# Kernel optimization log

Measured on AMD Instinct MI355X. Metric: run time of the kernel, lower is better.

Reference implementation:

```python
import jax, jax.numpy as jnp
import numpy as np

H, D_MODEL, TOPK = 8, 512, 32
D_K = D_MODEL // H


def setup_inputs() -> dict:
    key = jax.random.key(0)
    ks = jax.random.split(key, 12)
    B, LQ, LM = 8, 1024, 4096
    s = 1.0 / np.sqrt(D_MODEL)
    inp = {
        "query": jax.random.normal(ks[0], (B, LQ, D_MODEL), jnp.float32),
        "key": jax.random.normal(ks[1], (B, LM, D_MODEL), jnp.float32),
        "value": jax.random.normal(ks[2], (B, LM, D_MODEL), jnp.float32),
        "Wq": jax.random.normal(ks[3], (D_MODEL, D_MODEL), jnp.float32) * s,
        "bq": jax.random.normal(ks[4], (D_MODEL,), jnp.float32) * s,
        "Wk": jax.random.normal(ks[5], (D_MODEL, D_MODEL), jnp.float32) * s,
        "bk": jax.random.normal(ks[6], (D_MODEL,), jnp.float32) * s,
        "Wv": jax.random.normal(ks[7], (D_MODEL, D_MODEL), jnp.float32) * s,
        "bv": jax.random.normal(ks[8], (D_MODEL,), jnp.float32) * s,
        "Wo": jax.random.normal(ks[9], (D_MODEL, D_MODEL), jnp.float32) * s,
        "bo": jax.random.normal(ks[10], (D_MODEL,), jnp.float32) * s,
    }
    return inp


def reference(query, key, value, Wq, bq, Wk, bk, Wv, bv, Wo, bo):
    B, LQ, _ = query.shape
    LM = key.shape[1]
    # torch Linear: x @ W.T + b
    q = (query @ Wq.T + bq).reshape(B, LQ, H, D_K).transpose(0, 2, 1, 3)  # [B,H,LQ,Dk]
    k = (key @ Wk.T + bk).reshape(B, LM, H, D_K).transpose(0, 2, 1, 3)    # [B,H,LM,Dk]
    v = (value @ Wv.T + bv).reshape(B, LM, H, D_K).transpose(0, 2, 1, 3)  # [B,H,LM,Dk]

    scores = jnp.einsum("bhqd,bhmd->bhqm", q, k) / np.sqrt(D_K)          # [B,H,LQ,LM]
    sel_scores, idx = jax.lax.top_k(scores, TOPK)                          # [B,H,LQ,TOPK]
    # gather selected values: [B,H,LQ,TOPK,Dk]
    sel_v = jnp.take_along_axis(v[:, :, None, :, :], idx[..., None], axis=3)
    p_attn = jax.nn.softmax(sel_scores, axis=-1)                           # dropout: eval mode
    x = jnp.einsum("bhqt,bhqtd->bhqd", p_attn, sel_v)                      # [B,H,LQ,Dk]
    x = x.transpose(0, 2, 1, 3).reshape(B, LQ, H * D_K)
    return x @ Wo.T + bo
```

## Files before the change

### kernel.cpp

```cpp
#include <hip/hip_runtime.h>
#include <math.h>

#define DEV static __device__ __forceinline__

DEV void load8(const float* p, float* v) {
    float4 a = *(const float4*)p;
    float4 b = *(const float4*)(p + 4);
    v[0] = a.x; v[1] = a.y; v[2] = a.z; v[3] = a.w;
    v[4] = b.x; v[5] = b.y; v[6] = b.z; v[7] = b.w;
}

__global__ __launch_bounds__(256) void gemm_nt512(
    const float* __restrict__ A, const float* __restrict__ W,
    const float* __restrict__ bias, float* __restrict__ C)
{
    constexpr int BK = 32, NK = 512;
    __shared__ float As[BK][64 + 4];
    __shared__ float Bs[BK][64 + 4];
    const int bm = blockIdx.y * 64, bn = blockIdx.x * 64;
    const int tid = threadIdx.x;
    const int tx = tid & 15, ty = tid >> 4;
    const int lr = tid >> 2, lk = (tid & 3) * 8;
    float acc[4][4] = {};

    for (int k0 = 0; k0 < NK; k0 += BK) {
        float va[8], vb[8];
        load8(A + (size_t)(bm + lr) * NK + k0 + lk, va);
        load8(W + (size_t)(bn + lr) * NK + k0 + lk, vb);
#pragma unroll
        for (int i = 0; i < 8; ++i) { As[lk + i][lr] = va[i]; Bs[lk + i][lr] = vb[i]; }
        __syncthreads();
#pragma unroll
        for (int kk = 0; kk < BK; ++kk) {
            float4 a4 = *(const float4*)&As[kk][ty * 4];
            float4 b4 = *(const float4*)&Bs[kk][tx * 4];
            float a[4] = {a4.x, a4.y, a4.z, a4.w};
            float b[4] = {b4.x, b4.y, b4.z, b4.w};
#pragma unroll
            for (int i = 0; i < 4; ++i)
#pragma unroll
                for (int j = 0; j < 4; ++j)
                    acc[i][j] = fmaf(a[i], b[j], acc[i][j]);
        }
        __syncthreads();
    }

    float4 bv = *(const float4*)&bias[bn + tx * 4];
    float bvv[4] = {bv.x, bv.y, bv.z, bv.w};
#pragma unroll
    for (int i = 0; i < 4; ++i) {
        size_t row = (size_t)(bm + ty * 4 + i) * NK + bn + tx * 4;
        float4 o;
        o.x = acc[i][0] + bvv[0];
        o.y = acc[i][1] + bvv[1];
        o.z = acc[i][2] + bvv[2];
        o.w = acc[i][3] + bvv[3];
        *(float4*)&C[row] = o;
    }
}

__global__ __launch_bounds__(256) void topk_attn_fused(
    const float* __restrict__ Qf, const float* __restrict__ Kf,
    const float* __restrict__ Vp, float* __restrict__ Xp)
{
    constexpr int LQ = 1024, LM = 4096, DK = 64, D = 512, QT = 32, MT = 64, TK = 32, T = 24;
    __shared__ __align__(16) char smem[17408 + 8704 + 9216];
    float  (*ks)[68]   = (float  (*)[68])(smem);
    float  (*wsel)[33] = (float  (*)[33])(smem);
    int    (*isel)[33] = (int    (*)[33])(smem + 4224);
    float  (*qs)[68]   = (float  (*)[68])(smem + 17408);
    float  (*sc)[72]   = (float  (*)[72])(smem + 17408 + 8704);

    const int tid  = threadIdx.x;
    const int lane = tid & 63;
    const int w    = tid >> 6;
    const int g    = lane >> 3, j = lane & 7;
    const int r    = 8 * w + g;
    const int qt = blockIdx.x, h = blockIdx.y, b = blockIdx.z;

    {
        int rr = tid >> 3, d0 = (tid & 7) * 8;
        const float* src = Qf + ((size_t)(b * LQ + qt * QT + rr) * D + h * DK + d0);
        float4 a = *(const float4*)src;
        float4 c = *(const float4*)(src + 4);
        *(float4*)&qs[rr][d0]     = a;
        *(float4*)&qs[rr][d0 + 4] = c;
    }

    float bv[T]; int bi[T];
#pragma unroll
    for (int t = 0; t < T; ++t) { bv[t] = -INFINITY; bi[t] = 0; }
    float curmin = -INFINITY; int minpos = 0;

    const int qg = tid >> 5, mg = tid & 31;
    __syncthreads();

#pragma unroll 1
    for (int mc = 0; mc < LM; mc += MT) {
        {
            int rr = tid >> 2, d0 = (tid & 3) * 16;
            const float* src = Kf + ((size_t)(b * LM + mc + rr) * D + h * DK + d0);
#pragma unroll
            for (int i = 0; i < 16; i += 4)
                *(float4*)&ks[rr][d0 + i] = *(const float4*)(src + i);
        }
        __syncthreads();

        float acc[4][2] = {};
#pragma unroll
        for (int d = 0; d < DK; d += 4) {
            float4 qa[4], kb[2];
#pragma unroll
            for (int i = 0; i < 4; ++i) qa[i] = *(const float4*)&qs[qg + 8 * i][d];
#pragma unroll
            for (int jj = 0; jj < 2; ++jj) kb[jj] = *(const float4*)&ks[mg + 32 * jj][d];
#pragma unroll
            for (int i = 0; i < 4; ++i)
#pragma unroll
                for (int jj = 0; jj < 2; ++jj) {
                    acc[i][jj] = fmaf(qa[i].x, kb[jj].x, acc[i][jj]);
                    acc[i][jj] = fmaf(qa[i].y, kb[jj].y, acc[i][jj]);
                    acc[i][jj] = fmaf(qa[i].z, kb[jj].z, acc[i][jj]);
                    acc[i][jj] = fmaf(qa[i].w, kb[jj].w, acc[i][jj]);
                }
        }
#pragma unroll
        for (int i = 0; i < 4; ++i)
#pragma unroll
            for (int jj = 0; jj < 2; ++jj)
                sc[qg + 8 * i][mg + 32 * jj] = acc[i][jj] * 0.125f;
        __syncthreads();

#pragma unroll
        for (int c = 0; c < 8; ++c) {
            float v = sc[r][8 * c + j];
            if (v > curmin) {
                int idx = mc + 8 * c + j;
#pragma unroll
                for (int t = 0; t < T; ++t)
                    if (t == minpos) { bv[t] = v; bi[t] = idx; }
                float mv = bv[0]; int mp = 0;
#pragma unroll
                for (int t = 1; t < T; ++t)
                    if (bv[t] < mv) { mv = bv[t]; mp = t; }
                curmin = mv; minpos = mp;
            }
        }
        __syncthreads();
    }

    unsigned cons = 0;
    float m0 = 0.0f;
    double sum_part = 0.0;
#pragma unroll 1
    for (int t32 = 0; t32 < TK; ++t32) {
        float lm = -INFINITY; int li = 0x7fffffff; int lp = -1;
#pragma unroll
        for (int t = 0; t < T; ++t) {
            bool ok = !(cons & (1u << t));
            if (ok && (bv[t] > lm || (bv[t] == lm && bi[t] < li))) {
                lm = bv[t]; li = bi[t]; lp = t;
            }
        }
        float gv = lm; int gi = li;
#pragma unroll
        for (int k = 1; k < 8; k <<= 1) {
            float ov = __shfl_xor(gv, k);
            int   oi = __shfl_xor(gi, k);
            if (ov > gv || (ov == gv && oi < gi)) { gv = ov; gi = oi; }
        }
        if (lp >= 0 && gv == lm && gi == li) cons |= 1u << lp;
        if (t32 == 0) m0 = gv;
        if ((t32 & 7) == j) {
            double e = exp((double)(gv - m0));
            sum_part += e;
            isel[r][t32] = gi;
            wsel[r][t32] = (float)e;
        }
    }
#pragma unroll
    for (int k = 1; k < 8; k <<= 1) sum_part += __shfl_xor(sum_part, k);
    {
        double inv = 1.0 / sum_part;
#pragma unroll
        for (int tt = 0; tt < 4; ++tt) {
            int t = 8 * tt + j;
            wsel[r][t] = (float)((double)wsel[r][t] * inv);
        }
    }
    __syncthreads();

    {
        int rr = tid >> 3, d0 = (tid & 7) * 8;
        float4 a0 = {0, 0, 0, 0}, a1 = {0, 0, 0, 0};
#pragma unroll 1
        for (int t = 0; t < TK; ++t) {
            float ww = wsel[rr][t];
            int mi   = isel[rr][t];
            const float* vp = Vp + ((size_t)(b * LM + mi) * D + h * DK + d0);
            float4 v0 = *(const float4*)vp;
            float4 v1 = *(const float4*)(vp + 4);
            a0.x = fmaf(ww, v0.x, a0.x); a0.y = fmaf(ww, v0.y, a0.y);
            a0.z = fmaf(ww, v0.z, a0.z); a0.w = fmaf(ww, v0.w, a0.w);
            a1.x = fmaf(ww, v1.x, a1.x); a1.y = fmaf(ww, v1.y, a1.y);
            a1.z = fmaf(ww, v1.z, a1.z); a1.w = fmaf(ww, v1.w, a1.w);
        }
        float* xp = Xp + ((size_t)(b * LQ + qt * QT + rr) * D + h * DK + d0);
        *(float4*)xp       = a0;
        *(float4*)(xp + 4) = a1;
    }
}

extern "C" void kernel_launch(void* const* d_in, const int* in_sizes, int n_in,
                              void* d_out, int out_size, void* d_ws, size_t ws_size,
                              hipStream_t stream) {
    const float* query = (const float*)d_in[0];
    const float* key   = (const float*)d_in[1];
    const float* value = (const float*)d_in[2];
    const float* Wq    = (const float*)d_in[3];
    const float* bq    = (const float*)d_in[4];
    const float* Wk    = (const float*)d_in[5];
    const float* bk    = (const float*)d_in[6];
    const float* Wv    = (const float*)d_in[7];
    const float* bv    = (const float*)d_in[8];
    const float* Wo    = (const float*)d_in[9];
    const float* bo    = (const float*)d_in[10];
    float* out = (float*)d_out;

    float* Vp = (float*)d_ws;
    float* Xp = Vp + (size_t)32768 * 512;
    float* Qf = Xp + (size_t)8192 * 512;
    float* Kf = Qf + (size_t)8192 * 512;

    dim3 blk(256);
    gemm_nt512<<<dim3(8, 128), blk, 0, stream>>>(query, Wq, bq, Qf);
    gemm_nt512<<<dim3(8, 512), blk, 0, stream>>>(key,   Wk, bk, Kf);
    gemm_nt512<<<dim3(8, 512), blk, 0, stream>>>(value, Wv, bv, Vp);
    topk_attn_fused<<<dim3(32, 8, 8), blk, 0, stream>>>(Qf, Kf, Vp, Xp);
    gemm_nt512<<<dim3(8, 128), blk, 0, stream>>>(Xp, Wo, bo, out);
}
```

Before: 2.077 ms.

## Read Q via wave-uniform scalar loads and double key tile per iteration

```diff
diff --git a/kernel.cpp b/kernel.cpp
--- a/kernel.cpp
+++ b/kernel.cpp
@@ -63,13 +63,12 @@
     const float* __restrict__ Qf, const float* __restrict__ Kf,
     const float* __restrict__ Vp, float* __restrict__ Xp)
 {
-    constexpr int LQ = 1024, LM = 4096, DK = 64, D = 512, QT = 32, MT = 64, TK = 32, T = 24;
-    __shared__ __align__(16) char smem[17408 + 8704 + 9216];
-    float  (*ks)[68]   = (float  (*)[68])(smem);
-    float  (*wsel)[33] = (float  (*)[33])(smem);
-    int    (*isel)[33] = (int    (*)[33])(smem + 4224);
-    float  (*qs)[68]   = (float  (*)[68])(smem + 17408);
-    float  (*sc)[72]   = (float  (*)[72])(smem + 17408 + 8704);
+    constexpr int LQ = 1024, LM = 4096, DK = 64, D = 512, QT = 32, MT = 128, TK = 32, T = 24;
+    __shared__ __align__(16) char smem[34816];
+    float (*ks)[68]    = (float (*)[68])(smem);
+    float (*sc)[136]   = (float (*)[136])(smem + 17408);
+    float (*wsel)[33]  = (float (*)[33])(smem);
+    int   (*isel)[33]  = (int   (*)[33])(smem + 4224);
 
     const int tid  = threadIdx.x;
     const int lane = tid & 63;
@@ -78,61 +77,58 @@
     const int r    = 8 * w + g;
     const int qt = blockIdx.x, h = blockIdx.y, b = blockIdx.z;
 
-    {
-        int rr = tid >> 3, d0 = (tid & 7) * 8;
-        const float* src = Qf + ((size_t)(b * LQ + qt * QT + rr) * D + h * DK + d0);
-        float4 a = *(const float4*)src;
-        float4 c = *(const float4*)(src + 4);
-        *(float4*)&qs[rr][d0]     = a;
-        *(float4*)&qs[rr][d0 + 4] = c;
-    }
+    const int wu = __builtin_amdgcn_readfirstlane(w);
+    const float* qb = Qf + ((size_t)(b * LQ + qt * QT + 8 * wu) * D + h * DK);
 
     float bv[T]; int bi[T];
 #pragma unroll
     for (int t = 0; t < T; ++t) { bv[t] = -INFINITY; bi[t] = 0; }
     float curmin = -INFINITY; int minpos = 0;
 
-    const int qg = tid >> 5, mg = tid & 31;
-    __syncthreads();
+    const int srr = tid >> 2, sd0 = (tid & 3) * 16;
 
 #pragma unroll 1
     for (int mc = 0; mc < LM; mc += MT) {
-        {
-            int rr = tid >> 2, d0 = (tid & 3) * 16;
-            const float* src = Kf + ((size_t)(b * LM + mc + rr) * D + h * DK + d0);
-#pragma unroll
-            for (int i = 0; i < 16; i += 4)
-                *(float4*)&ks[rr][d0 + i] = *(const float4*)(src + i);
-        }
-        __syncthreads();
-
-        float acc[4][2] = {};
-#pragma unroll
-        for (int d = 0; d < DK; d += 4) {
-            float4 qa[4], kb[2];
-#pragma unroll
-            for (int i = 0; i < 4; ++i) qa[i] = *(const float4*)&qs[qg + 8 * i][d];
-#pragma unroll
-            for (int jj = 0; jj < 2; ++jj) kb[jj] = *(const float4*)&ks[mg + 32 * jj][d];
-#pragma unroll
-            for (int i = 0; i < 4; ++i)
-#pragma unroll
-                for (int jj = 0; jj < 2; ++jj) {
-                    acc[i][jj] = fmaf(qa[i].x, kb[jj].x, acc[i][jj]);
-                    acc[i][jj] = fmaf(qa[i].y, kb[jj].y, acc[i][jj]);
-                    acc[i][jj] = fmaf(qa[i].z, kb[jj].z, acc[i][jj]);
-                    acc[i][jj] = fmaf(qa[i].w, kb[jj].w, acc[i][jj]);
+#pragma unroll
+        for (int p = 0; p < 2; ++p) {
+            const float* src = Kf + ((size_t)(b * LM + mc + 64 * p + srr) * D + h * DK + sd0);
+#pragma unroll
+            for (int i2 = 0; i2 < 16; i2 += 4)
+                *(float4*)&ks[64 * p + srr][sd0 + i2] = *(const float4*)(src + i2);
+        }
+        __syncthreads();
+
+        float acc[8][2] = {};
+#pragma unroll 1
+        for (int dc = 0; dc < DK; dc += 4) {
+            float qv[8][4];
+#pragma unroll
+            for (int i = 0; i < 8; ++i)
+#pragma unroll
+                for (int dd = 0; dd < 4; ++dd)
+                    qv[i][dd] = qb[(size_t)i * D + dc + dd];
+            float k0[4], k1[4];
+            *(float4*)&k0[0] = *(const float4*)&ks[lane][dc];
+            *(float4*)&k1[0] = *(const float4*)&ks[64 + lane][dc];
+#pragma unroll
+            for (int dd = 0; dd < 4; ++dd)
+#pragma unroll
+                for (int i = 0; i < 8; ++i) {
+                    acc[i][0] = fmaf(qv[i][dd], k0[dd], acc[i][0]);
+                    acc[i][1] = fmaf(qv[i][dd], k1[dd], acc[i][1]);
                 }
         }
-#pragma unroll
-        for (int i = 0; i < 4; ++i)
-#pragma unroll
-            for (int jj = 0; jj < 2; ++jj)
-                sc[qg + 8 * i][mg + 32 * jj] = acc[i][jj] * 0.125f;
-        __syncthreads();
-
-#pragma unroll
-        for (int c = 0; c < 8; ++c) {
+        __syncthreads();
+
+#pragma unroll
+        for (int i = 0; i < 8; ++i) {
+            sc[8 * wu + i][lane]      = acc[i][0] * 0.125f;
+            sc[8 * wu + i][64 + lane] = acc[i][1] * 0.125f;
+        }
+        __syncthreads();
+
+#pragma unroll
+        for (int c = 0; c < 16; ++c) {
             float v = sc[r][8 * c + j];
             if (v > curmin) {
                 int idx = mc + 8 * c + j;
```

After: 2.307 ms. +11.0%, slower.

## Replace per-element top-k insertion with threshold filtering and candidate rescoring

Applied to the files above, without the earlier changes.

```diff
diff --git a/kernel.cpp b/kernel.cpp
--- a/kernel.cpp
+++ b/kernel.cpp
@@ -10,15 +10,12 @@
     v[4] = b.x; v[5] = b.y; v[6] = b.z; v[7] = b.w;
 }
 
-__global__ __launch_bounds__(256) void gemm_nt512(
-    const float* __restrict__ A, const float* __restrict__ W,
-    const float* __restrict__ bias, float* __restrict__ C)
+DEV void gemm_body(const float* __restrict__ A, const float* __restrict__ W,
+                   const float* __restrict__ bias, float* __restrict__ C,
+                   int bm, int bn, int tid,
+                   float (*As)[68], float (*Bs)[68])
 {
     constexpr int BK = 32, NK = 512;
-    __shared__ float As[BK][64 + 4];
-    __shared__ float Bs[BK][64 + 4];
-    const int bm = blockIdx.y * 64, bn = blockIdx.x * 64;
-    const int tid = threadIdx.x;
     const int tx = tid & 15, ty = tid >> 4;
     const int lr = tid >> 2, lk = (tid & 3) * 8;
     float acc[4][4] = {};
@@ -45,8 +42,8 @@
         __syncthreads();
     }
 
-    float4 bv = *(const float4*)&bias[bn + tx * 4];
-    float bvv[4] = {bv.x, bv.y, bv.z, bv.w};
+    float4 bvv4 = *(const float4*)&bias[bn + tx * 4];
+    float bvv[4] = {bvv4.x, bvv4.y, bvv4.z, bvv4.w};
 #pragma unroll
     for (int i = 0; i < 4; ++i) {
         size_t row = (size_t)(bm + ty * 4 + i) * NK + bn + tx * 4;
@@ -59,17 +56,45 @@
     }
 }
 
+__global__ __launch_bounds__(256) void gemm_nt512(
+    const float* __restrict__ A, const float* __restrict__ W,
+    const float* __restrict__ bias, float* __restrict__ C)
+{
+    __shared__ float As[32][68];
+    __shared__ float Bs[32][68];
+    gemm_body(A, W, bias, C, blockIdx.y * 64, blockIdx.x * 64, threadIdx.x, As, Bs);
+}
+
+__global__ __launch_bounds__(256) void gemm_qkv(
+    const float* __restrict__ Aq, const float* __restrict__ Ak, const float* __restrict__ Av,
+    const float* __restrict__ Wq, const float* __restrict__ Wk, const float* __restrict__ Wv,
+    const float* __restrict__ bq, const float* __restrict__ bk, const float* __restrict__ bv,
+    float* __restrict__ Cq, float* __restrict__ Ck, float* __restrict__ Cv)
+{
+    __shared__ float As[32][68];
+    __shared__ float Bs[32][68];
+    int yb = blockIdx.y;
+    const float *A, *W, *bias; float* C; int bm;
+    if (yb < 128)      { A = Aq; W = Wq; bias = bq; C = Cq; bm = yb * 64; }
+    else if (yb < 640) { A = Ak; W = Wk; bias = bk; C = Ck; bm = (yb - 128) * 64; }
+    else               { A = Av; W = Wv; bias = bv; C = Cv; bm = (yb - 640) * 64; }
+    gemm_body(A, W, bias, C, bm, blockIdx.x * 64, threadIdx.x, As, Bs);
+}
+
 __global__ __launch_bounds__(256) void topk_attn_fused(
     const float* __restrict__ Qf, const float* __restrict__ Kf,
-    const float* __restrict__ Vp, float* __restrict__ Xp)
+    const float* __restrict__ Vp, float* __restrict__ Xp,
+    unsigned short* __restrict__ gbuf)
 {
-    constexpr int LQ = 1024, LM = 4096, DK = 64, D = 512, QT = 32, MT = 64, TK = 32, T = 24;
-    __shared__ __align__(16) char smem[17408 + 8704 + 9216];
-    float  (*ks)[68]   = (float  (*)[68])(smem);
-    float  (*wsel)[33] = (float  (*)[33])(smem);
-    int    (*isel)[33] = (int    (*)[33])(smem + 4224);
-    float  (*qs)[68]   = (float  (*)[68])(smem + 17408);
-    float  (*sc)[72]   = (float  (*)[72])(smem + 17408 + 8704);
+    constexpr int LQ = 1024, LM = 4096, DK = 64, D = 512, QT = 32, MT = 256, TK = 32, T = 24;
+    constexpr int CAP = 624;
+    __shared__ __align__(16) char smem[69632 + 8704 + 128];
+    float (*ks)[68]   = (float (*)[68])(smem);
+    float (*sc)[264]  = (float (*)[264])(smem + 34816);
+    float (*wsel)[33] = (float (*)[33])(smem);
+    int   (*isel)[33] = (int   (*)[33])(smem + 4224);
+    float (*qs)[68]   = (float (*)[68])(smem + 69632);
+    int*  cnt         = (int*)(smem + 69632 + 8704);
 
     const int tid  = threadIdx.x;
     const int lane = tid & 63;
@@ -77,6 +102,8 @@
     const int g    = lane >> 3, j = lane & 7;
     const int r    = 8 * w + g;
     const int qt = blockIdx.x, h = blockIdx.y, b = blockIdx.z;
+
+    const size_t bb = ((size_t)(((b * 8) + h) * 32 + qt) * 32 + r) * CAP;
 
     {
         int rr = tid >> 3, d0 = (tid & 7) * 8;
@@ -86,67 +113,110 @@
         *(float4*)&qs[rr][d0]     = a;
         *(float4*)&qs[rr][d0 + 4] = c;
     }
-
-    float bv[T]; int bi[T];
-#pragma unroll
-    for (int t = 0; t < T; ++t) { bv[t] = -INFINITY; bi[t] = 0; }
-    float curmin = -INFINITY; int minpos = 0;
-
-    const int qg = tid >> 5, mg = tid & 31;
+    if (tid < 32) cnt[tid] = 0;
+
+    float s0 = -INFINITY, s1 = -INFINITY, s2 = -INFINITY, s3 = -INFINITY;
+    float tau = -INFINITY;
+
+    const int qy = tid >> 5, tx = tid & 31;
+    const int srr = tid >> 2, sd0 = (tid & 3) * 16;
     __syncthreads();
 
 #pragma unroll 1
     for (int mc = 0; mc < LM; mc += MT) {
-        {
-            int rr = tid >> 2, d0 = (tid & 3) * 16;
-            const float* src = Kf + ((size_t)(b * LM + mc + rr) * D + h * DK + d0);
-#pragma unroll
-            for (int i = 0; i < 16; i += 4)
-                *(float4*)&ks[rr][d0 + i] = *(const float4*)(src + i);
-        }
-        __syncthreads();
-
-        float acc[4][2] = {};
-#pragma unroll
-        for (int d = 0; d < DK; d += 4) {
-            float4 qa[4], kb[2];
-#pragma unroll
-            for (int i = 0; i < 4; ++i) qa[i] = *(const float4*)&qs[qg + 8 * i][d];
-#pragma unroll
-            for (int jj = 0; jj < 2; ++jj) kb[jj] = *(const float4*)&ks[mg + 32 * jj][d];
+#pragma unroll
+        for (int p = 0; p < 4; ++p) {
+            const float* src = Kf + ((size_t)(b * LM + mc + 64 * p + srr) * D + h * DK + sd0);
+#pragma unroll
+            for (int i2 = 0; i2 < 16; i2 += 4)
+                *(float4*)&ks[64 * p + srr][sd0 + i2] = *(const float4*)(src + i2);
+        }
+        __syncthreads();
+
+        float acc[4][8] = {};
+#pragma unroll 2
+        for (int dc = 0; dc < DK; dc += 4) {
+            float4 qa[4], kb[8];
+#pragma unroll
+            for (int i = 0; i < 4; ++i) qa[i] = *(const float4*)&qs[qy + 8 * i][dc];
+#pragma unroll
+            for (int jj = 0; jj < 8; ++jj) kb[jj] = *(const float4*)&ks[tx + 32 * jj][dc];
 #pragma unroll
             for (int i = 0; i < 4; ++i)
 #pragma unroll
-                for (int jj = 0; jj < 2; ++jj) {
+                for (int jj = 0; jj < 8; ++jj) {
                     acc[i][jj] = fmaf(qa[i].x, kb[jj].x, acc[i][jj]);
                     acc[i][jj] = fmaf(qa[i].y, kb[jj].y, acc[i][jj]);
                     acc[i][jj] = fmaf(qa[i].z, kb[jj].z, acc[i][jj]);
                     acc[i][jj] = fmaf(qa[i].w, kb[jj].w, acc[i][jj]);
                 }
         }
+        __syncthreads();
+
 #pragma unroll
         for (int i = 0; i < 4; ++i)
 #pragma unroll
-            for (int jj = 0; jj < 2; ++jj)
-                sc[qg + 8 * i][mg + 32 * jj] = acc[i][jj] * 0.125f;
-        __syncthreads();
-
-#pragma unroll
-        for (int c = 0; c < 8; ++c) {
+            for (int jj = 0; jj < 8; ++jj)
+                sc[qy + 8 * i][tx + 32 * jj] = acc[i][jj] * 0.125f;
+        __syncthreads();
+
+#pragma unroll 8
+        for (int c = 0; c < 32; ++c) {
             float v = sc[r][8 * c + j];
-            if (v > curmin) {
-                int idx = mc + 8 * c + j;
-#pragma unroll
-                for (int t = 0; t < T; ++t)
-                    if (t == minpos) { bv[t] = v; bi[t] = idx; }
-                float mv = bv[0]; int mp = 0;
-#pragma unroll
-                for (int t = 1; t < T; ++t)
-                    if (bv[t] < mv) { mv = bv[t]; mp = t; }
-                curmin = mv; minpos = mp;
+            if (v > s3) {
+                if (v > s0)      { s3 = s2; s2 = s1; s1 = s0; s0 = v; }
+                else if (v > s1) { s3 = s2; s2 = s1; s1 = v; }
+                else if (v > s2) { s3 = s2; s2 = v; }
+                else             { s3 = v; }
             }
-        }
-        __syncthreads();
+            if (v > tau) {
+                int pos = atomicAdd(&cnt[r], 1);
+                if (pos < CAP) gbuf[bb + pos] = (unsigned short)(mc + 8 * c + j);
+            }
+            if ((c & 7) == 7) {
+                float t4 = s3;
+                t4 = fminf(t4, __shfl_xor(t4, 1));
+                t4 = fminf(t4, __shfl_xor(t4, 2));
+                t4 = fminf(t4, __shfl_xor(t4, 4));
+                tau = t4;
+            }
+        }
+        __syncthreads();
+    }
+
+    const int nc = min(cnt[r], CAP);
+    float bv[T]; int bi[T];
+#pragma unroll
+    for (int t = 0; t < T; ++t) { bv[t] = -INFINITY; bi[t] = 0; }
+    float curmin = -INFINITY; int minpos = 0, minidx = 0;
+
+#pragma unroll 1
+    for (int p = j; p < nc; p += 8) {
+        int idx = gbuf[bb + p];
+        const float* krow = Kf + ((size_t)(b * LM + idx) * D + h * DK);
+        float a = 0.0f;
+#pragma unroll
+        for (int d = 0; d < DK; d += 4) {
+            float4 k4 = *(const float4*)(krow + d);
+            float4 q4 = *(const float4*)&qs[r][d];
+            a = fmaf(q4.x, k4.x, a);
+            a = fmaf(q4.y, k4.y, a);
+            a = fmaf(q4.z, k4.z, a);
+            a = fmaf(q4.w, k4.w, a);
+        }
+        float v = a * 0.125f;
+
+        bool take = (v > curmin) || (v == curmin && idx < minidx);
+        if (take) {
+#pragma unroll
+            for (int t = 0; t < T; ++t)
+                if (t == minpos) { bv[t] = v; bi[t] = idx; }
+            float mv = bv[0]; int mp = 0, mi = bi[0];
+#pragma unroll
+            for (int t = 1; t < T; ++t)
+                if (bv[t] < mv || (bv[t] == mv && bi[t] > mi)) { mv = bv[t]; mp = t; mi = bi[t]; }
+            curmin = mv; minpos = mp; minidx = mi;
+        }
     }
 
     unsigned cons = 0;
@@ -231,11 +301,12 @@
     float* Xp = Vp + (size_t)32768 * 512;
     float* Qf = Xp + (size_t)8192 * 512;
     float* Kf = Qf + (size_t)8192 * 512;
+    unsigned short* gbuf = (unsigned short*)((char*)d_ws + (size_t)167772160);
 
     dim3 blk(256);
-    gemm_nt512<<<dim3(8, 128), blk, 0, stream>>>(query, Wq, bq, Qf);
-    gemm_nt512<<<dim3(8, 512), blk, 0, stream>>>(key,   Wk, bk, Kf);
-    gemm_nt512<<<dim3(8, 512), blk, 0, stream>>>(value, Wv, bv, Vp);
-    topk_attn_fused<<<dim3(32, 8, 8), blk, 0, stream>>>(Qf, Kf, Vp, Xp);
+    gemm_qkv<<<dim3(8, 1152), blk, 0, stream>>>(query, key, value,
+                                                Wq, Wk, Wv, bq, bk, bv,
+                                                Qf, Kf, Vp);
+    topk_attn_fused<<<dim3(32, 8, 8), blk, 0, stream>>>(Qf, Kf, Vp, Xp, gbuf);
     gemm_nt512<<<dim3(8, 128), blk, 0, stream>>>(Xp, Wo, bo, out);
 }
```

After: 2.410 ms. +16.0%, slower.
